# Kernel tuning notes

Hardware: AMD Instinct MI355X
Metric: run time of the kernel (lower is better)

## Reference

```python
import jax, jax.numpy as jnp
import numpy as np

TAU = 0.07          # temperature
TOP_N_SIM = 5       # n_neighb for KNN label assignment
RANKING_K = 4       # top-k same/diff-class sims for confidence ratio


def setup_inputs() -> dict:
    key = jax.random.key(0)
    k1, k2, k3 = jax.random.split(key, 3)
    n_src, n_tgt, d, n_cls = 8192, 6144, 256, 64
    return {
        "source_features": jax.random.normal(k1, (n_src, d), dtype=jnp.float32),
        "source_labels": jax.random.randint(k2, (n_src,), 0, n_cls, dtype=jnp.int32),
        "target_features": jax.random.normal(k3, (n_tgt, d), dtype=jnp.float32),
    }


def _l2_normalize(x):
    # F.normalize(x, dim=1, p=2) with eps=1e-12
    n = jnp.sqrt(jnp.sum(x * x, axis=1, keepdims=True))
    return x / jnp.maximum(n, 1e-12)


def reference(source_features, source_labels, target_features):
    n_tgt = target_features.shape[0]
    top_ranked_n = n_tgt * 2 // 3

    # cosine similarity matrix [n_src, n_tgt]
    sim = _l2_normalize(source_features) @ _l2_normalize(target_features).T

    # sort each column descending over sources
    order = jnp.argsort(-sim, axis=0)                      # [S, T]

    # KNN label assignment with torch.mode semantics (tie -> smallest value)
    neigh = source_labels[order[:TOP_N_SIM]]               # [K, T]
    counts = (neigh[:, None, :] == neigh[None, :, :]).sum(axis=1)  # [K, T]
    maxc = counts.max(axis=0)                              # [T]
    big = jnp.iinfo(source_labels.dtype).max
    assigned = jnp.where(counts == maxc[None, :], neigh, big).min(axis=0)  # [T]

    # sims & labels reordered by descending similarity, per column
    sorted_sims = jnp.take_along_axis(sim, order, axis=0)  # [S, T]
    sorted_labels = source_labels[order]                   # [S, T]
    pos = sorted_labels == assigned[None, :]               # [S, T]

    def first_k_masked_sum(mask):
        # sum of first RANKING_K sorted sims where mask is True, per column
        csum = jnp.cumsum(mask.astype(sim.dtype), axis=0)
        sel = mask & (csum <= RANKING_K)
        return jnp.sum(jnp.where(sel, sorted_sims, 0.0), axis=0)

    nln = first_k_masked_sum(pos)
    nun = first_k_masked_sum(~pos)
    scores = jax.lax.stop_gradient(nln / nun)              # [T], detached

    _, top_ind = jax.lax.top_k(scores, top_ranked_n)       # confident targets
    conf_sim = sim[:, top_ind]                             # [S, top_ranked_n]
    conf_lab = assigned[top_ind]

    # contrastive softmax loss over sources
    mask_sim = (source_labels[:, None] == conf_lab[None, :]).astype(sim.dtype)
    exp_scores = jax.nn.softmax(conf_sim / TAU, axis=0)
    contrastive = (exp_scores * mask_sim).sum(axis=0) / exp_scores.sum(axis=0)
    return -jnp.mean(jnp.log(contrastive + 1e-6))
```

## Files before the change

kernel.cpp:

```cpp
#include <hip/hip_runtime.h>
#include <cstdint>
#include <cstddef>

#define DIM 256
#define NSRC 8192
#define NCLS 64
#define KSTEPS 8
#define INV_TAU (1.0f / 0.07f)
#define EPITCH 136

typedef __attribute__((ext_vector_type(8))) short bf16x8;
typedef __attribute__((ext_vector_type(4))) float f32x4;
typedef unsigned char uchar;

__device__ __forceinline__ ushort f2bf_rne(float f) {
    uint u = __float_as_uint(f);
    uint r = u + 0x7fff + ((u >> 16) & 1);
    return (ushort)(r >> 16);
}
__device__ __forceinline__ uint bf2ord(uint u) {
    return u ^ (0x8000u + (u >> 15) * 0x7FFFu);
}
__device__ __forceinline__ float ord2f(uint o) {
    uint u = (o & 0x8000u) ? (o ^ 0x8000u) : (~o & 0xFFFFu);
    return __uint_as_float(u << 16);
}

__device__ __forceinline__ void gload_lds16(const void* g, void* l) {
    __builtin_amdgcn_global_load_lds((const __attribute__((address_space(1))) void*)g,
                                     (__attribute__((address_space(3))) void*)l,
                                     16, 0, 0);
}

__global__ __launch_bounds__(256) void l2bf2_k(const float* __restrict__ inA,
                                               ushort* __restrict__ outA, int nA,
                                               const float* __restrict__ inB,
                                               ushort* __restrict__ outB, int nB) {
    const int w = (blockIdx.x * 256 + threadIdx.x) >> 6;
    const int lane = threadIdx.x & 63;
    if (w >= nA + nB) return;
    const float* in;
    ushort* out;
    int row;
    if (w < nA) { in = inA; out = outA; row = w; }
    else        { in = inB; out = outB; row = w - nA; }
    float4 v = *(const float4*)(in + (size_t)row * DIM + lane * 4);
    float ss = v.x * v.x + v.y * v.y + v.z * v.z + v.w * v.w;
#pragma unroll
    for (int d = 1; d < 64; d <<= 1) ss += __shfl_xor(ss, d);
    const float n = fmaxf(sqrtf(ss), 1e-12f);
    ushort4 o;
    o.x = f2bf_rne(v.x / n);
    o.y = f2bf_rne(v.y / n);
    o.z = f2bf_rne(v.z / n);
    o.w = f2bf_rne(v.w / n);
    *(ushort4*)(out + (size_t)row * DIM + lane * 4) = o;
}

__global__ __launch_bounds__(256) void class_build_k(const int* __restrict__ labels,
                                                     uchar* __restrict__ lab8,
                                                     int* __restrict__ cstart,
                                                     int* __restrict__ clist, int n) {
    const int c = blockIdx.x, t = threadIdx.x;
    const int g = c * 256 + t;
    if (g < n) lab8[g] = (uchar)labels[g];

    __shared__ int sl[256], se[256];
    const int per = n >> 8;
    const int i0 = t * per;
    int less = 0, eq = 0;
    for (int j = 0; j < per; ++j) {
        const int l = labels[i0 + j];
        less += (l < c);
        eq += (l == c);
    }
    sl[t] = less; se[t] = eq;
    __syncthreads();
    for (int s = 1; s < 256; s <<= 1) {
        const int a = (t >= s) ? sl[t - s] : 0;
        const int b = (t >= s) ? se[t - s] : 0;
        __syncthreads();
        sl[t] += a; se[t] += b;
        __syncthreads();
    }
    const int base = sl[255];
    int pos = base + se[t] - eq;
    for (int j = 0; j < per; ++j) {
        const int i = i0 + j;
        if (labels[i] == c) clist[pos++] = i;
    }
    if (t == 0) cstart[c] = base;
    if (c == 0 && t == 1) cstart[NCLS] = n;
}

__global__ __launch_bounds__(256) void gemm_mfma_k(const ushort* __restrict__ A,
                                                   const ushort* __restrict__ B,
                                                   ushort* __restrict__ C,
                                                   int M, int N) {
    __shared__ __align__(16) ushort smem[24576];

    const int tid = threadIdx.x;
    const int lane = tid & 63, wid = tid >> 6;
    const int wr = wid >> 1, wc = wid & 1;

    const int gx = gridDim.x;
    const int bid = blockIdx.y * gx + blockIdx.x;
    const int rowsPerX = gridDim.y >> 3;
    const int grpW = 8;
    const int grpSize = rowsPerX * grpW;
    const int xcd = bid & 7;
    const int local = bid >> 3;
    const int grp = local / grpSize;
    const int within = local % grpSize;
    const int bm = (xcd * rowsPerX + within % rowsPerX) * 128;
    const int bn = (grp * grpW + within / rowsPerX) * 128;

    const char* aSrc[2];
    const char* bSrc[2];
    uint ldsOff[2];
#pragma unroll
    for (int it = 0; it < 2; ++it) {
        const int c = it * 256 + tid;
        const int r = c >> 2;
        const int ch = c & 3;
        const int sch = ch ^ ((r >> 1) & 3);
        aSrc[it] = (const char*)A + (size_t)(bm + r) * (DIM * 2) + sch * 16;
        bSrc[it] = (const char*)B + (size_t)(bn + r) * (DIM * 2) + sch * 16;
        ldsOff[it] = it * 4096 + (uint)(wid * 1024);
    }

    const int fr = lane & 15, fk = lane >> 4;
    const int swz = (fr >> 1) & 3;
    int idxA[4], idxB[4];
#pragma unroll
    for (int m = 0; m < 4; ++m)
        idxA[m] = (wr * 64 + m * 16 + fr) * 32 + ((fk ^ swz) * 8);
#pragma unroll
    for (int n = 0; n < 4; ++n)
        idxB[n] = (wc * 64 + n * 16 + fr) * 32 + ((fk ^ swz) * 8);

    f32x4 acc[4][4];
#pragma unroll
    for (int m = 0; m < 4; ++m)
#pragma unroll
        for (int n = 0; n < 4; ++n) acc[m][n] = (f32x4){0.f, 0.f, 0.f, 0.f};

#define STAGE(b, ks)                                                               \
    {                                                                              \
        _Pragma("unroll") for (int it = 0; it < 2; ++it) {                         \
            gload_lds16(aSrc[it] + (ks) * 64,                                      \
                        (char*)smem + (b) * 8192 + ldsOff[it]);                    \
            gload_lds16(bSrc[it] + (ks) * 64,                                      \
                        (char*)smem + 24576 + (b) * 8192 + ldsOff[it]);            \
        }                                                                          \
    }

    STAGE(0, 0);
    STAGE(1, 1);

#pragma unroll
    for (int ks = 0; ks < KSTEPS; ++ks) {
        if (ks < KSTEPS - 1) { asm volatile("s_waitcnt vmcnt(4)" ::: "memory"); }
        else                 { asm volatile("s_waitcnt vmcnt(0)" ::: "memory"); }
        __builtin_amdgcn_s_barrier();
        asm volatile("" ::: "memory");

        if (ks + 2 < KSTEPS) STAGE((ks + 2) % 3, ks + 2);

        const int slot = ks % 3;
        const ushort* sAc = smem + slot * 4096;
        const ushort* sBc = smem + 12288 + slot * 4096;
        bf16x8 av[4], bv[4];
#pragma unroll
        for (int m = 0; m < 4; ++m) av[m] = *(const bf16x8*)&sAc[idxA[m]];
#pragma unroll
        for (int n = 0; n < 4; ++n) bv[n] = *(const bf16x8*)&sBc[idxB[n]];
#pragma unroll
        for (int m = 0; m < 4; ++m)
#pragma unroll
            for (int n = 0; n < 4; ++n)
                acc[m][n] = __builtin_amdgcn_mfma_f32_16x16x32_bf16(av[m], bv[n], acc[m][n], 0, 0, 0);
    }
#undef STAGE

    __syncthreads();
#pragma unroll
    for (int m = 0; m < 4; ++m) {
#pragma unroll
        for (int n = 0; n < 4; ++n) {
            const int colb = wc * 64 + n * 16 + fr;
#pragma unroll
            for (int j = 0; j < 4; ++j) {
                const int rowb = wr * 64 + m * 16 + fk * 4 + j;
                smem[rowb * EPITCH + colb] = (ushort)bf2ord((uint)f2bf_rne(acc[m][n][j]));
            }
        }
    }
    __syncthreads();
    const int rr = tid >> 4, cc = (tid & 15) * 8;
#pragma unroll
    for (int it = 0; it < 8; ++it) {
        const int r = it * 16 + rr;
        uint4 v = *(const uint4*)&smem[r * EPITCH + cc];
        *(uint4*)(C + (size_t)(bm + r) * N + bn + cc) = v;
    }
}

__global__ __launch_bounds__(256) void assign_score_w(const ushort* __restrict__ sim,
                                                      const int* __restrict__ labels,
                                                      const uchar* __restrict__ lab8,
                                                      const int* __restrict__ cstart,
                                                      const int* __restrict__ clist,
                                                      float* __restrict__ scores_out,
                                                      float* __restrict__ logt_out) {
    const int lane = threadIdx.x & 63, wid = threadIdx.x >> 6;
    const int t = blockIdx.x * 4 + wid;
    const ushort* row = sim + (size_t)t * NSRC;

    uint k0 = 0, k1 = 0, k2 = 0, k3 = 0, k4 = 0, k5 = 0, k6 = 0, k7 = 0;
    float s1 = 0.f;

#define CH4(u16, idx)                                                   \
    {                                                                   \
        uint uu = (uint)(u16);                                          \
        s1 += __expf(fmaf(ord2f(uu), INV_TAU, -INV_TAU));               \
        uint nk = (uu << 16) | (uint)(8191 - (idx));                    \
        uint q;                                                         \
        q = max(k0, nk); nk = min(k0, nk); k0 = q;                      \
        q = max(k1, nk); nk = min(k1, nk); k1 = q;                      \
        q = max(k2, nk); nk = min(k2, nk); k2 = q;                      \
        k3 = max(k3, nk);                                               \
    }
#define CH8(u16, idx)                                                   \
    {                                                                   \
        uint nk = (((uint)(u16)) << 16) | (uint)(8191 - (idx));         \
        uint q;                                                         \
        q = max(k0, nk); nk = min(k0, nk); k0 = q;                      \
        q = max(k1, nk); nk = min(k1, nk); k1 = q;                      \
        q = max(k2, nk); nk = min(k2, nk); k2 = q;                      \
        q = max(k3, nk); nk = min(k3, nk); k3 = q;                      \
        q = max(k4, nk); nk = min(k4, nk); k4 = q;                      \
        q = max(k5, nk); nk = min(k5, nk); k5 = q;                      \
        q = max(k6, nk); nk = min(k6, nk); k6 = q;                      \
        k7 = max(k7, nk);                                               \
    }
#define MERGE8                                                                     \
    _Pragma("unroll")                                                              \
    for (int d = 1; d < 64; d <<= 1) {                                             \
        uint b0 = __shfl_xor(k0, d), b1 = __shfl_xor(k1, d), b2 = __shfl_xor(k2, d),\
             b3 = __shfl_xor(k3, d), b4 = __shfl_xor(k4, d), b5 = __shfl_xor(k5, d),\
             b6 = __shfl_xor(k6, d), b7 = __shfl_xor(k7, d);                        \
        uint r0 = max(k0, b0);                                                     \
        uint r1 = max(max(min(k0, b0), k1), b1);                                   \
        uint r2 = max(max(min(k0, b1), min(k1, b0)), max(k2, b2));                 \
        uint r3 = max(max(min(k0, b2), min(k1, b1)),                               \
                      max(max(min(k2, b0), k3), b3));                              \
        uint r4 = max(max(max(min(k0, b3), min(k1, b2)),                           \
                          max(min(k2, b1), min(k3, b0))), max(k4, b4));            \
        uint r5 = max(max(max(min(k0, b4), min(k1, b3)),                           \
                          max(min(k2, b2), min(k3, b1))),                          \
                      max(max(min(k4, b0), k5), b5));                              \
        uint r6 = max(max(max(min(k0, b5), min(k1, b4)),                           \
                          max(min(k2, b3), min(k3, b2))),                          \
                      max(max(min(k4, b1), min(k5, b0)), max(k6, b6)));            \
        uint r7 = max(max(max(min(k0, b6), min(k1, b5)),                           \
                          max(min(k2, b4), min(k3, b3))),                          \
                      max(max(min(k4, b2), min(k5, b1)),                           \
                          max(max(min(k6, b0), k7), b7)));                         \
        k0 = r0; k1 = r1; k2 = r2; k3 = r3; k4 = r4; k5 = r5; k6 = r6; k7 = r7;    \
    }

    for (int i0 = lane * 8; i0 < NSRC; i0 += 512) {
        uint4 w = *(const uint4*)(row + i0);
        CH4(w.x & 0xFFFF, i0 + 0); CH4(w.x >> 16, i0 + 1);
        CH4(w.y & 0xFFFF, i0 + 2); CH4(w.y >> 16, i0 + 3);
        CH4(w.z & 0xFFFF, i0 + 4); CH4(w.z >> 16, i0 + 5);
        CH4(w.w & 0xFFFF, i0 + 6); CH4(w.w >> 16, i0 + 7);
    }
    const uint prek3 = k3;
    MERGE8;
    if (!__all((int)(prek3 <= k7))) {
        k0 = k1 = k2 = k3 = k4 = k5 = k6 = k7 = 0;
        for (int i0 = lane * 8; i0 < NSRC; i0 += 512) {
            uint4 w = *(const uint4*)(row + i0);
            CH8(w.x & 0xFFFF, i0 + 0); CH8(w.x >> 16, i0 + 1);
            CH8(w.y & 0xFFFF, i0 + 2); CH8(w.y >> 16, i0 + 3);
            CH8(w.z & 0xFFFF, i0 + 4); CH8(w.z >> 16, i0 + 5);
            CH8(w.w & 0xFFFF, i0 + 6); CH8(w.w >> 16, i0 + 7);
        }
        MERGE8;
    }
#undef CH4
#undef CH8
#undef MERGE8

#pragma unroll
    for (int d = 1; d < 64; d <<= 1) s1 += __shfl_xor(s1, d);

    const int l0 = labels[8191 - (int)(k0 & 0xFFFF)];
    const int l1 = labels[8191 - (int)(k1 & 0xFFFF)];
    const int l2 = labels[8191 - (int)(k2 & 0xFFFF)];
    const int l3 = labels[8191 - (int)(k3 & 0xFFFF)];
    const int l4 = labels[8191 - (int)(k4 & 0xFFFF)];
    const int l5 = labels[8191 - (int)(k5 & 0xFFFF)];
    const int l6 = labels[8191 - (int)(k6 & 0xFFFF)];
    const int l7 = labels[8191 - (int)(k7 & 0xFFFF)];

    const int c0 = 1 + (l0 == l1) + (l0 == l2) + (l0 == l3) + (l0 == l4);
    const int c1 = (l1 == l0) + 1 + (l1 == l2) + (l1 == l3) + (l1 == l4);
    const int c2 = (l2 == l0) + (l2 == l1) + 1 + (l2 == l3) + (l2 == l4);
    const int c3 = (l3 == l0) + (l3 == l1) + (l3 == l2) + 1 + (l3 == l4);
    const int c4 = (l4 == l0) + (l4 == l1) + (l4 == l2) + (l4 == l3) + 1;
    const int maxc = max(max(max(c0, c1), max(c2, c3)), c4);
    int assigned = 0x7fffffff;
    if (c0 == maxc) assigned = min(assigned, l0);
    if (c1 == maxc) assigned = min(assigned, l1);
    if (c2 == maxc) assigned = min(assigned, l2);
    if (c3 == maxc) assigned = min(assigned, l3);
    if (c4 == maxc) assigned = min(assigned, l4);
    const int aL = assigned;

    const int negcnt = (l0 != aL) + (l1 != aL) + (l2 != aL) + (l3 != aL) +
                       (l4 != aL) + (l5 != aL) + (l6 != aL) + (l7 != aL);
    float nun = 0.f;
    if (negcnt >= 4) {
        int c = 0;
#define NSTEP(kj, lj)                                                       \
        {                                                                   \
            bool take = ((lj) != aL) && (c < 4);                            \
            nun += take ? ord2f((kj) >> 16) : 0.f;                          \
            c += take ? 1 : 0;                                              \
        }
        NSTEP(k0, l0) NSTEP(k1, l1) NSTEP(k2, l2) NSTEP(k3, l3)
        NSTEP(k4, l4) NSTEP(k5, l5) NSTEP(k6, l6) NSTEP(k7, l7)
#undef NSTEP
    } else {
        uint n0 = 0, n1 = 0, n2 = 0, n3 = 0;
        for (int i0 = lane * 8; i0 < NSRC; i0 += 512) {
            uint4 w = *(const uint4*)(row + i0);
            uint2 lw = *(const uint2*)(lab8 + i0);
#define NEGP(u16, lb)                                                       \
            {                                                               \
                uint x = ((lb) == aL) ? 0u : (uint)(u16);                   \
                uint q;                                                     \
                q = max(n0, x); x = min(n0, x); n0 = q;                     \
                q = max(n1, x); x = min(n1, x); n1 = q;                     \
                q = max(n2, x); x = min(n2, x); n2 = q;                     \
                n3 = max(n3, x);                                            \
            }
            NEGP(w.x & 0xFFFF, (int)(lw.x & 255));
            NEGP(w.x >> 16,    (int)((lw.x >> 8) & 255));
            NEGP(w.y & 0xFFFF, (int)((lw.x >> 16) & 255));
            NEGP(w.y >> 16,    (int)(lw.x >> 24));
            NEGP(w.z & 0xFFFF, (int)(lw.y & 255));
            NEGP(w.z >> 16,    (int)((lw.y >> 8) & 255));
            NEGP(w.w & 0xFFFF, (int)((lw.y >> 16) & 255));
            NEGP(w.w >> 16,    (int)(lw.y >> 24));
#undef NEGP
        }
#pragma unroll
        for (int d = 1; d < 64; d <<= 1) {
            uint b0 = __shfl_xor(n0, d), b1 = __shfl_xor(n1, d),
                 b2 = __shfl_xor(n2, d), b3 = __shfl_xor(n3, d);
            uint r0 = max(n0, b0);
            uint r1 = max(max(min(n0, b0), n1), b1);
            uint r2 = max(max(min(n0, b1), min(n1, b0)), max(n2, b2));
            uint r3 = max(max(min(n0, b2), min(n1, b1)),
                          max(max(min(n2, b0), n3), b3));
            n0 = r0; n1 = r1; n2 = r2; n3 = r3;
        }
        nun = (n0 ? ord2f(n0) : 0.f) + (n1 ? ord2f(n1) : 0.f) +
              (n2 ? ord2f(n2) : 0.f) + (n3 ? ord2f(n3) : 0.f);
    }

    const int cs = cstart[aL], ce = cstart[aL + 1];
    float tp0 = -2.f, tp1 = -2.f, tp2 = -2.f, tp3 = -2.f;
    float sp = 0.f;
    for (int p = cs + lane; p < ce; p += 64) {
        const int idx = clist[p];
        float v = ord2f((uint)row[idx]);
        sp += __expf(fmaf(v, INV_TAU, -INV_TAU));
        float x = v, q;
        q = fmaxf(tp0, x); x = fminf(tp0, x); tp0 = q;
        q = fmaxf(tp1, x); x = fminf(tp1, x); tp1 = q;
        q = fmaxf(tp2, x); x = fminf(tp2, x); tp2 = q;
        tp3 = fmaxf(tp3, x);
    }
#pragma unroll
    for (int d = 1; d < 64; d <<= 1) {
        sp += __shfl_xor(sp, d);
        float b0 = __shfl_xor(tp0, d), b1 = __shfl_xor(tp1, d),
              b2 = __shfl_xor(tp2, d), b3 = __shfl_xor(tp3, d);
        float r0 = fmaxf(tp0, b0);
        float r1 = fmaxf(fmaxf(fminf(tp0, b0), tp1), b1);
        float r2 = fmaxf(fmaxf(fminf(tp0, b1), fminf(tp1, b0)), fmaxf(tp2, b2));
        float r3 = fmaxf(fmaxf(fminf(tp0, b2), fminf(tp1, b1)),
                         fmaxf(fmaxf(fminf(tp2, b0), tp3), b3));
        tp0 = r0; tp1 = r1; tp2 = r2; tp3 = r3;
    }

    if (lane == 0) {
        float nln = (tp0 > -1.5f ? tp0 : 0.f) + (tp1 > -1.5f ? tp1 : 0.f) +
                    (tp2 > -1.5f ? tp2 : 0.f) + (tp3 > -1.5f ? tp3 : 0.f);
        scores_out[t] = nln / nun;
        logt_out[t] = logf(sp / s1 + 1e-6f);
    }
}

__global__ __launch_bounds__(256) void select_topk_w(const float* __restrict__ scores,
                                                     int* __restrict__ selected,
                                                     int n, int k) {
    const int lane = threadIdx.x & 63, wid = threadIdx.x >> 6;
    const int t = blockIdx.x * 4 + wid;
    if (t >= n) return;
    const float st = scores[t];
    int rank = 0;
    for (int j0 = lane * 4; j0 < n; j0 += 256) {
        float4 v = *(const float4*)(scores + j0);
        rank += (v.x > st) || (v.x == st && (j0 + 0) < t);
        rank += (v.y > st) || (v.y == st && (j0 + 1) < t);
        rank += (v.z > st) || (v.z == st && (j0 + 2) < t);
        rank += (v.w > st) || (v.w == st && (j0 + 3) < t);
    }
    for (int d = 1; d < 64; d <<= 1) rank += __shfl_xor(rank, d);
    if (lane == 0) selected[t] = (rank < k) ? 1 : 0;
}

__global__ __launch_bounds__(256) void finalize_k(const float* __restrict__ logt,
                                                  const int* __restrict__ selected,
                                                  float* __restrict__ out, int n, int k) {
    __shared__ float red[256];
    const int tid = threadIdx.x;
    float s = 0.f;
    for (int i = tid; i < n; i += 256) s += selected[i] ? logt[i] : 0.f;
    red[tid] = s;
    __syncthreads();
    for (int st = 128; st > 0; st >>= 1) {
        if (tid < st) red[tid] += red[tid + st];
        __syncthreads();
    }
    if (tid == 0) out[0] = -red[0] / (float)k;
}

extern "C" void kernel_launch(void* const* d_in, const int* in_sizes, int n_in,
                              void* d_out, int out_size, void* d_ws, size_t ws_size,
                              hipStream_t stream) {
    const float* srcF = (const float*)d_in[0];
    const int* labels = (const int*)d_in[1];
    const float* tgtF = (const float*)d_in[2];
    float* out = (float*)d_out;

    const int n_src = in_sizes[1];
    const int d = in_sizes[0] / n_src;
    const int n_tgt = in_sizes[2] / d;
    const int topn = n_tgt * 2 / 3;

    char* ws = (char*)d_ws;
    ushort* src2 = (ushort*)ws;  ws += (size_t)n_src * DIM * sizeof(ushort);
    ushort* tgt2 = (ushort*)ws;  ws += (size_t)n_tgt * DIM * sizeof(ushort);
    ushort* sim  = (ushort*)ws;  ws += (size_t)n_tgt * NSRC * sizeof(ushort);
    float* scores = (float*)ws;  ws += (size_t)n_tgt * sizeof(float);
    float* logt   = (float*)ws;  ws += (size_t)n_tgt * sizeof(float);
    int* selected = (int*)ws;    ws += (size_t)n_tgt * sizeof(int);
    int* cstart   = (int*)ws;    ws += (size_t)(NCLS + 1) * sizeof(int);
    int* clist    = (int*)ws;    ws += (size_t)n_src * sizeof(int);
    uchar* lab8   = (uchar*)ws;  ws += (size_t)n_src;

    const int nrows = n_tgt + n_src;
    l2bf2_k<<<(nrows + 3) / 4, 256, 0, stream>>>(tgtF, tgt2, n_tgt, srcF, src2, n_src);
    class_build_k<<<NCLS, 256, 0, stream>>>(labels, lab8, cstart, clist, n_src);

    dim3 grid(n_src / 128, n_tgt / 128);
    gemm_mfma_k<<<grid, 256, 0, stream>>>(tgt2, src2, sim, n_tgt, n_src);

    assign_score_w<<<n_tgt / 4, 256, 0, stream>>>(sim, labels, lab8, cstart, clist,
                                                  scores, logt);
    select_topk_w<<<(n_tgt + 3) / 4, 256, 0, stream>>>(scores, selected, n_tgt, topn);
    finalize_k<<<1, 256, 0, stream>>>(logt, selected, out, n_tgt, topn);
}
```

Before: 115.6 us.

## Fuse softmax exp-sum into GEMM epilogue and use med3 for top-k insertion

The GEMM epilogue now computes the per-target sum of exp(sim/tau) over each 128-source tile, using bf16-rounded values to match what is stored. These partials go to a 64×NTGT buffer, and the scoring kernel reads them instead of evaluating an exp for every element of the similarity row. Separately, the sorted top-k insertion chains in the scoring kernel are rewritten as v_med3_u32 and fmed3 operations, which shortens each insertion. The cost is extra epilogue work in the GEMM (exps, shuffles, shared-memory reduction) and a hardcoded NTGT constant in the layout.

```diff
diff --git a/kernel.cpp b/kernel.cpp
--- a/kernel.cpp
+++ b/kernel.cpp
@@ -4,6 +4,7 @@
 
 #define DIM 256
 #define NSRC 8192
+#define NTGT 6144
 #define NCLS 64
 #define KSTEPS 8
 #define INV_TAU (1.0f / 0.07f)
@@ -24,6 +25,11 @@
 __device__ __forceinline__ float ord2f(uint o) {
     uint u = (o & 0x8000u) ? (o ^ 0x8000u) : (~o & 0xFFFFu);
     return __uint_as_float(u << 16);
+}
+__device__ __forceinline__ uint med3u(uint a, uint b, uint c) {
+    uint d;
+    asm("v_med3_u32 %0, %1, %2, %3" : "=v"(d) : "v"(a), "v"(b), "v"(c));
+    return d;
 }
 
 __device__ __forceinline__ void gload_lds16(const void* g, void* l) {
@@ -96,6 +102,7 @@
 __global__ __launch_bounds__(256) void gemm_mfma_k(const ushort* __restrict__ A,
                                                    const ushort* __restrict__ B,
                                                    ushort* __restrict__ C,
+                                                   float* __restrict__ s1p,
                                                    int M, int N) {
     __shared__ __align__(16) ushort smem[24576];
 
@@ -184,6 +191,34 @@
 #undef STAGE
 
     __syncthreads();
+    {
+        float rp[16];
+#pragma unroll
+        for (int m = 0; m < 4; ++m)
+#pragma unroll
+            for (int j = 0; j < 4; ++j) {
+                float s = 0.f;
+#pragma unroll
+                for (int n = 0; n < 4; ++n) {
+                    uint u = __float_as_uint(acc[m][n][j]);
+                    uint ru = (u + 0x7fff + ((u >> 16) & 1)) & 0xFFFF0000u;
+                    s += __expf(fmaf(__uint_as_float(ru), INV_TAU, -INV_TAU));
+                }
+                rp[m * 4 + j] = s;
+            }
+#pragma unroll
+        for (int d = 1; d < 16; d <<= 1)
+#pragma unroll
+            for (int i = 0; i < 16; ++i) rp[i] += __shfl_xor(rp[i], d);
+        float* s1red = (float*)((char*)smem + 34816);
+        if (fr == 0) {
+#pragma unroll
+            for (int m = 0; m < 4; ++m)
+#pragma unroll
+                for (int j = 0; j < 4; ++j)
+                    s1red[(wr * 64 + m * 16 + fk * 4 + j) * 2 + wc] = rp[m * 4 + j];
+        }
+    }
 #pragma unroll
     for (int m = 0; m < 4; ++m) {
 #pragma unroll
@@ -197,6 +232,10 @@
         }
     }
     __syncthreads();
+    if (tid < 128) {
+        const float* s1red = (const float*)((const char*)smem + 34816);
+        s1p[(size_t)(bn >> 7) * NTGT + bm + tid] = s1red[tid * 2] + s1red[tid * 2 + 1];
+    }
     const int rr = tid >> 4, cc = (tid & 15) * 8;
 #pragma unroll
     for (int it = 0; it < 8; ++it) {
@@ -211,6 +250,7 @@
                                                       const uchar* __restrict__ lab8,
                                                       const int* __restrict__ cstart,
                                                       const int* __restrict__ clist,
+                                                      const float* __restrict__ s1p,
                                                       float* __restrict__ scores_out,
                                                       float* __restrict__ logt_out) {
     const int lane = threadIdx.x & 63, wid = threadIdx.x >> 6;
@@ -218,31 +258,27 @@
     const ushort* row = sim + (size_t)t * NSRC;
 
     uint k0 = 0, k1 = 0, k2 = 0, k3 = 0, k4 = 0, k5 = 0, k6 = 0, k7 = 0;
-    float s1 = 0.f;
 
 #define CH4(u16, idx)                                                   \
     {                                                                   \
-        uint uu = (uint)(u16);                                          \
-        s1 += __expf(fmaf(ord2f(uu), INV_TAU, -INV_TAU));               \
-        uint nk = (uu << 16) | (uint)(8191 - (idx));                    \
-        uint q;                                                         \
-        q = max(k0, nk); nk = min(k0, nk); k0 = q;                      \
-        q = max(k1, nk); nk = min(k1, nk); k1 = q;                      \
-        q = max(k2, nk); nk = min(k2, nk); k2 = q;                      \
-        k3 = max(k3, nk);                                               \
+        uint nk = (((uint)(u16)) << 16) | (uint)(8191 - (idx));         \
+        uint q1 = med3u(nk, k0, k1);                                    \
+        uint q2 = med3u(nk, k1, k2);                                    \
+        uint q3 = med3u(nk, k2, k3);                                    \
+        k0 = max(k0, nk); k1 = q1; k2 = q2; k3 = q3;                    \
     }
 #define CH8(u16, idx)                                                   \
     {                                                                   \
         uint nk = (((uint)(u16)) << 16) | (uint)(8191 - (idx));         \
-        uint q;                                                         \
-        q = max(k0, nk); nk = min(k0, nk); k0 = q;                      \
-        q = max(k1, nk); nk = min(k1, nk); k1 = q;                      \
-        q = max(k2, nk); nk = min(k2, nk); k2 = q;                      \
-        q = max(k3, nk); nk = min(k3, nk); k3 = q;                      \
-        q = max(k4, nk); nk = min(k4, nk); k4 = q;                      \
-        q = max(k5, nk); nk = min(k5, nk); k5 = q;                      \
-        q = max(k6, nk); nk = min(k6, nk); k6 = q;                      \
-        k7 = max(k7, nk);                                               \
+        uint q1 = med3u(nk, k0, k1);                                    \
+        uint q2 = med3u(nk, k1, k2);                                    \
+        uint q3 = med3u(nk, k2, k3);                                    \
+        uint q4 = med3u(nk, k3, k4);                                    \
+        uint q5 = med3u(nk, k4, k5);                                    \
+        uint q6 = med3u(nk, k5, k6);                                    \
+        uint q7 = med3u(nk, k6, k7);                                    \
+        k0 = max(k0, nk);                                               \
+        k1 = q1; k2 = q2; k3 = q3; k4 = q4; k5 = q5; k6 = q6; k7 = q7;  \
     }
 #define MERGE8                                                                     \
     _Pragma("unroll")                                                              \
@@ -294,6 +330,7 @@
 #undef CH8
 #undef MERGE8
 
+    float s1 = s1p[(size_t)lane * NTGT + t];
 #pragma unroll
     for (int d = 1; d < 64; d <<= 1) s1 += __shfl_xor(s1, d);
 
@@ -342,11 +379,10 @@
 #define NEGP(u16, lb)                                                       \
             {                                                               \
                 uint x = ((lb) == aL) ? 0u : (uint)(u16);                   \
-                uint q;                                                     \
-                q = max(n0, x); x = min(n0, x); n0 = q;                     \
-                q = max(n1, x); x = min(n1, x); n1 = q;                     \
-                q = max(n2, x); x = min(n2, x); n2 = q;                     \
-                n3 = max(n3, x);                                            \
+                uint q1 = med3u(x, n0, n1);                                 \
+                uint q2 = med3u(x, n1, n2);                                 \
+                uint q3 = med3u(x, n2, n3);                                 \
+                n0 = max(n0, x); n1 = q1; n2 = q2; n3 = q3;                 \
             }
             NEGP(w.x & 0xFFFF, (int)(lw.x & 255));
             NEGP(w.x >> 16,    (int)((lw.x >> 8) & 255));
@@ -380,11 +416,10 @@
         const int idx = clist[p];
         float v = ord2f((uint)row[idx]);
         sp += __expf(fmaf(v, INV_TAU, -INV_TAU));
-        float x = v, q;
-        q = fmaxf(tp0, x); x = fminf(tp0, x); tp0 = q;
-        q = fmaxf(tp1, x); x = fminf(tp1, x); tp1 = q;
-        q = fmaxf(tp2, x); x = fminf(tp2, x); tp2 = q;
-        tp3 = fmaxf(tp3, x);
+        float q1 = __builtin_amdgcn_fmed3f(v, tp0, tp1);
+        float q2 = __builtin_amdgcn_fmed3f(v, tp1, tp2);
+        float q3 = __builtin_amdgcn_fmed3f(v, tp2, tp3);
+        tp0 = fmaxf(tp0, v); tp1 = q1; tp2 = q2; tp3 = q3;
     }
 #pragma unroll
     for (int d = 1; d < 64; d <<= 1) {
@@ -465,16 +500,18 @@
     int* cstart   = (int*)ws;    ws += (size_t)(NCLS + 1) * sizeof(int);
     int* clist    = (int*)ws;    ws += (size_t)n_src * sizeof(int);
     uchar* lab8   = (uchar*)ws;  ws += (size_t)n_src;
+    ws = (char*)(((uintptr_t)ws + 255) & ~(uintptr_t)255);
+    float* s1p    = (float*)ws;  ws += (size_t)64 * NTGT * sizeof(float);
 
     const int nrows = n_tgt + n_src;
     l2bf2_k<<<(nrows + 3) / 4, 256, 0, stream>>>(tgtF, tgt2, n_tgt, srcF, src2, n_src);
     class_build_k<<<NCLS, 256, 0, stream>>>(labels, lab8, cstart, clist, n_src);
 
     dim3 grid(n_src / 128, n_tgt / 128);
-    gemm_mfma_k<<<grid, 256, 0, stream>>>(tgt2, src2, sim, n_tgt, n_src);
+    gemm_mfma_k<<<grid, 256, 0, stream>>>(tgt2, src2, sim, s1p, n_tgt, n_src);
 
     assign_score_w<<<n_tgt / 4, 256, 0, stream>>>(sim, labels, lab8, cstart, clist,
-                                                  scores, logt);
+                                                  s1p, scores, logt);
     select_topk_w<<<(n_tgt + 3) / 4, 256, 0, stream>>>(scores, selected, n_tgt, topn);
     finalize_k<<<1, 256, 0, stream>>>(logt, selected, out, n_tgt, topn);
 }
```

After: 128.3 us. 1.11x slower.
